# Kernel optimization log

Hardware: AMD Instinct MI355X
Metric: run time of the kernel (lower is better)

Reference implementation:

```python
import jax, jax.numpy as jnp
import numpy as np

B, SQ, SK, D, H = 4, 2048, 2048, 1024, 16
EPS = 1e-6  # flax LayerNorm default


def layer_norm(x, g, b):
    m = x.mean(-1, keepdims=True)
    var = ((x - m) ** 2).mean(-1, keepdims=True)
    return (x - m) * jax.lax.rsqrt(var + EPS) * g + b


def setup_inputs() -> dict:
    key = jax.random.key(0)
    ks = jax.random.split(key, 16)
    s = 1.0 / np.sqrt(D).astype(np.float32)
    inp = {
        'q': jax.random.normal(ks[0], (B, SQ, D), jnp.float32),
        'k': jax.random.normal(ks[1], (B, SK, D), jnp.float32),
        'v': jax.random.normal(ks[2], (B, SK, D), jnp.float32),
        'mask': jax.random.randint(ks[3], (B, SK), 0, 2).astype(bool),
        'Wq': jax.random.normal(ks[4], (D, D), jnp.float32) * s,
        'bq': jnp.zeros((D,), jnp.float32),
        'Wk': jax.random.normal(ks[5], (D, D), jnp.float32) * s,
        'bk': jnp.zeros((D,), jnp.float32),
        'Wv': jax.random.normal(ks[6], (D, D), jnp.float32) * s,
        'bv': jnp.zeros((D,), jnp.float32),
        'Wo': jax.random.normal(ks[7], (D, D), jnp.float32) * s,
        'bo': jnp.zeros((D,), jnp.float32),
        'g1': jnp.ones((D,), jnp.float32),
        'b1': jnp.zeros((D,), jnp.float32),
        'g2': jnp.ones((D,), jnp.float32),
        'b2': jnp.zeros((D,), jnp.float32),
    }
    return inp


def reference(q, k, v, mask, Wq, bq, Wk, bk, Wv, bv, Wo, bo, g1, b1, g2, b2):
    qp = q @ Wq + bq                      # [B, SQ, D]
    kp = k @ Wk + bk                      # [B, SK, D]
    vp = v @ Wv + bv
    qh = qp.reshape(B, SQ, H, D // H)     # head = slice of last dim (matches scatter)
    kh = kp.reshape(B, SK, H, D // H)
    vh = vp.reshape(B, SK, H, D // H)
    # NOTE: original scales by sqrt(dim_out) (full dim), not head dim
    logits = jnp.einsum('bqhd,bkhd->bhqk', qh, kh) / np.sqrt(D).astype(np.float32)
    m = mask[:, None, None, :]            # [B,1,1,SK] broadcast over heads & queries
    A = jax.nn.softmax(jnp.where(m, logits, -jnp.inf), axis=-1)
    A = jnp.where(jnp.isnan(A), 0.0, A)   # fully-masked rows -> 0 (as in original)
    attn = jnp.einsum('bhqk,bkhd->bqhd', A, vh).reshape(B, SQ, D)  # gather heads
    x = layer_norm(qp + attn, g1, b1)
    out = layer_norm(x + jax.nn.relu(x @ Wo + bo), g2, b2)
    return out
```

## Files before the change

kernel.cpp:

```cpp
#include <hip/hip_runtime.h>

#define B_   4
#define SQS  2048
#define SKS  2048
#define DM   1024
#define H_   16
#define MT   8192

typedef __attribute__((ext_vector_type(8))) short bf16x8;
typedef __attribute__((ext_vector_type(4))) float f32x4;

__device__ __forceinline__ float bf2f(unsigned int u) { return __uint_as_float(u << 16); }
__device__ __forceinline__ unsigned short f2bf(float f) {
  unsigned int u = __float_as_uint(f);
  return (unsigned short)((u + 0x7fffu + ((u >> 16) & 1u)) >> 16);
}
__device__ __forceinline__ unsigned int pk_trunc(float a, float b) {
  return __builtin_amdgcn_perm(__float_as_uint(b), __float_as_uint(a), 0x07060302u);
}
__device__ __forceinline__ float fexp2(float x) {
#if __has_builtin(__builtin_amdgcn_exp2f)
  return __builtin_amdgcn_exp2f(x);
#else
  return __expf(x * 0.69314718056f);
#endif
}
__device__ __forceinline__ void async16(const void* g, void* l) {
  __builtin_amdgcn_global_load_lds((const __attribute__((address_space(1))) unsigned int*)g,
                                   (__attribute__((address_space(3))) unsigned int*)l,
                                   16, 0, 0);
}

#define KSCALE 0.0450842200f
#define BIAS_UNMASKED 0.0028151213f

__global__ __launch_bounds__(256)
void cvt3_kernel(const float* __restrict__ a, const float* __restrict__ b,
                 const float* __restrict__ c,
                 unsigned short* __restrict__ oa, unsigned short* __restrict__ ob,
                 unsigned short* __restrict__ oc)
{
  const float* src = (blockIdx.y == 0) ? a : (blockIdx.y == 1) ? b : c;
  unsigned short* dst = (blockIdx.y == 0) ? oa : (blockIdx.y == 1) ? ob : oc;
  size_t i = ((size_t)blockIdx.x * 256 + threadIdx.x) * 4;
  float4 f = *(const float4*)(src + i);
  uint2 o;
  o.x = (unsigned)f2bf(f.x) | ((unsigned)f2bf(f.y) << 16);
  o.y = (unsigned)f2bf(f.z) | ((unsigned)f2bf(f.w) << 16);
  *(uint2*)(dst + i) = o;
}

__global__ __launch_bounds__(256)
void wtrans_kernel(const float* __restrict__ w0, const float* __restrict__ w1,
                   const float* __restrict__ w2, const float* __restrict__ w3,
                   unsigned short* __restrict__ t0, unsigned short* __restrict__ t1,
                   unsigned short* __restrict__ t2, unsigned short* __restrict__ t3)
{
  const float* W = (blockIdx.z == 0) ? w0 : (blockIdx.z == 1) ? w1 : (blockIdx.z == 2) ? w2 : w3;
  unsigned short* Wt = (blockIdx.z == 0) ? t0 : (blockIdx.z == 1) ? t1 : (blockIdx.z == 2) ? t2 : t3;
  __shared__ float s[32][33];
  int n0 = blockIdx.x * 32, k0 = blockIdx.y * 32;
  int tid = threadIdx.x;
#pragma unroll
  for (int p = 0; p < 4; p++) {
    int idx = p * 256 + tid;
    int r = idx >> 5, c = idx & 31;
    s[r][c] = W[(size_t)(k0 + r) * DM + n0 + c];
  }
  __syncthreads();
#pragma unroll
  for (int p = 0; p < 4; p++) {
    int idx = p * 256 + tid;
    int r = idx >> 5, c = idx & 31;
    Wt[(size_t)(n0 + r) * DM + k0 + c] = f2bf(s[c][r]);
  }
}

__global__ __launch_bounds__(256)
void mkbias_kernel(const int* __restrict__ m, float* __restrict__ bias)
{
  int i = blockIdx.x * 256 + threadIdx.x;
  bias[i] = m[i] ? BIAS_UNMASKED : -1e30f;
}

__global__ __launch_bounds__(256)
void qkv_gemm(const unsigned short* __restrict__ A0, const unsigned short* __restrict__ A1,
              const unsigned short* __restrict__ A2,
              const unsigned short* __restrict__ W0, const unsigned short* __restrict__ W1,
              const unsigned short* __restrict__ W2,
              const float* __restrict__ s0, const float* __restrict__ s1,
              const float* __restrict__ s2,
              unsigned short* __restrict__ o0, unsigned short* __restrict__ o1,
              unsigned short* __restrict__ o2)
{
  const int L = blockIdx.x + (blockIdx.y << 3) + (blockIdx.z << 9);
  const int g = L & 7, i5 = L >> 3;
  const int nblk = i5 & 7;
  const int yz = (i5 >> 3) + g * 24;
  const int mblk = yz & 63;
  const int z = yz >> 6;

  const unsigned short* A  = (z == 0) ? A0 : (z == 1) ? A1 : A2;
  const unsigned short* Wt = (z == 0) ? W0 : (z == 1) ? W1 : W2;
  const float* bias        = (z == 0) ? s0 : (z == 1) ? s1 : s2;
  unsigned short* C        = (z == 0) ? o0 : (z == 1) ? o1 : o2;
  const float sc           = (z == 1) ? KSCALE : 1.0f;

  __shared__ short As[128 * 64];
  __shared__ short Bs[128 * 64];
  const int tid = threadIdx.x;
  const int m0 = mblk * 128, n0 = nblk * 128;
  const int wave = tid >> 6, ln = tid & 15, qd = (tid & 63) >> 4;
  const int wm = (wave >> 1) * 64, wn = (wave & 1) * 64;

  int srow[4], sgj[4];
#pragma unroll
  for (int u = 0; u < 4; u++) {
    int c = u * 256 + tid;
    srow[u] = c >> 3;
    sgj[u] = ((c & 7) ^ (srow[u] & 7)) * 8;
  }

  f32x4 acc[4][4];
  const f32x4 vzero = {0.f, 0.f, 0.f, 0.f};
#pragma unroll
  for (int i = 0; i < 4; i++)
#pragma unroll
    for (int j = 0; j < 4; j++) acc[i][j] = vzero;

  for (int k0 = 0; k0 < DM; k0 += 64) {
    __syncthreads();
#pragma unroll
    for (int u = 0; u < 4; u++) {
      int c = u * 256 + tid;
      async16(A  + (size_t)(m0 + srow[u]) * DM + k0 + sgj[u], (char*)As + c * 16);
      async16(Wt + (size_t)(n0 + srow[u]) * DM + k0 + sgj[u], (char*)Bs + c * 16);
    }
    __syncthreads();

#pragma unroll
    for (int kk = 0; kk < 2; kk++) {
      const int ch = ((kk * 4 + qd) ^ (ln & 7)) * 8;
      bf16x8 af[4], bfr[4];
#pragma unroll
      for (int i = 0; i < 4; i++)
        af[i] = *(const bf16x8*)(As + (wm + i * 16 + ln) * 64 + ch);
#pragma unroll
      for (int j = 0; j < 4; j++)
        bfr[j] = *(const bf16x8*)(Bs + (wn + j * 16 + ln) * 64 + ch);
#pragma unroll
      for (int i = 0; i < 4; i++)
#pragma unroll
        for (int j = 0; j < 4; j++)
          acc[i][j] = __builtin_amdgcn_mfma_f32_16x16x32_bf16(af[i], bfr[j], acc[i][j], 0, 0, 0);
    }
  }

#pragma unroll
  for (int j = 0; j < 4; j++) {
    int col = n0 + wn + j * 16 + ln;
    float bj = bias[col];
#pragma unroll
    for (int i = 0; i < 4; i++) {
      int row = m0 + wm + i * 16 + qd * 4;
#pragma unroll
      for (int r = 0; r < 4; r++)
        C[(size_t)(row + r) * DM + col] = f2bf((acc[i][j][r] + bj) * sc);
    }
  }
}

__global__ __launch_bounds__(256)
void gemm_bf16(const unsigned short* __restrict__ A,
               const unsigned short* __restrict__ Wt,
               const float* __restrict__ bias,
               unsigned short* __restrict__ C,
               int relu)
{
  const int L = blockIdx.x + (blockIdx.y << 3);
  const int g = L & 7, i5 = L >> 3;
  const int nblk = i5 & 7;
  const int mblk = (i5 >> 3) + (g << 3);

  __shared__ short As[128 * 64];
  __shared__ short Bs[128 * 64];
  const int tid = threadIdx.x;
  const int m0 = mblk * 128, n0 = nblk * 128;
  const int wave = tid >> 6, ln = tid & 15, qd = (tid & 63) >> 4;
  const int wm = (wave >> 1) * 64, wn = (wave & 1) * 64;

  int srow[4], sgj[4];
#pragma unroll
  for (int u = 0; u < 4; u++) {
    int c = u * 256 + tid;
    srow[u] = c >> 3;
    sgj[u] = ((c & 7) ^ (srow[u] & 7)) * 8;
  }

  f32x4 acc[4][4];
  const f32x4 vzero = {0.f, 0.f, 0.f, 0.f};
#pragma unroll
  for (int i = 0; i < 4; i++)
#pragma unroll
    for (int j = 0; j < 4; j++) acc[i][j] = vzero;

  for (int k0 = 0; k0 < DM; k0 += 64) {
    __syncthreads();
#pragma unroll
    for (int u = 0; u < 4; u++) {
      int c = u * 256 + tid;
      async16(A  + (size_t)(m0 + srow[u]) * DM + k0 + sgj[u], (char*)As + c * 16);
      async16(Wt + (size_t)(n0 + srow[u]) * DM + k0 + sgj[u], (char*)Bs + c * 16);
    }
    __syncthreads();

#pragma unroll
    for (int kk = 0; kk < 2; kk++) {
      const int ch = ((kk * 4 + qd) ^ (ln & 7)) * 8;
      bf16x8 af[4], bfr[4];
#pragma unroll
      for (int i = 0; i < 4; i++)
        af[i] = *(const bf16x8*)(As + (wm + i * 16 + ln) * 64 + ch);
#pragma unroll
      for (int j = 0; j < 4; j++)
        bfr[j] = *(const bf16x8*)(Bs + (wn + j * 16 + ln) * 64 + ch);
#pragma unroll
      for (int i = 0; i < 4; i++)
#pragma unroll
        for (int j = 0; j < 4; j++)
          acc[i][j] = __builtin_amdgcn_mfma_f32_16x16x32_bf16(af[i], bfr[j], acc[i][j], 0, 0, 0);
    }
  }

#pragma unroll
  for (int j = 0; j < 4; j++) {
    int col = n0 + wn + j * 16 + ln;
    float bj = bias[col];
#pragma unroll
    for (int i = 0; i < 4; i++) {
      int row = m0 + wm + i * 16 + qd * 4;
#pragma unroll
      for (int r = 0; r < 4; r++) {
        float v = acc[i][j][r] + bj;
        if (relu) v = fmaxf(v, 0.f);
        C[(size_t)(row + r) * DM + col] = f2bf(v);
      }
    }
  }
}

__global__ __launch_bounds__(256)
void vtrans_kernel(const unsigned short* __restrict__ vp, unsigned short* __restrict__ vT)
{
  __shared__ unsigned short s[64][68];
  int b = blockIdx.z, h = blockIdx.y, k0 = blockIdx.x * 64;
  int tid = threadIdx.x;
#pragma unroll
  for (int p = 0; p < 4; p++) {
    int c = p * 256 + tid;
    int k = c >> 4, d0 = (c & 15) * 4;
    uint2 u = *(const uint2*)(vp + (size_t)(b * SKS + k0 + k) * DM + (h << 6) + d0);
    *(uint2*)(&s[k][d0]) = u;
  }
  __syncthreads();
#pragma unroll
  for (int p = 0; p < 4; p++) {
    int c = p * 256 + tid;
    int d = c >> 4, m = c & 15;
    int t  = ((m & 1) << 1) | (m >> 3);
    int qd = (m >> 1) & 3;
    int ks = t * 16 + qd * 4;
    unsigned short r0 = s[ks + 0][d];
    unsigned short r1 = s[ks + 1][d];
    unsigned short r2 = s[ks + 2][d];
    unsigned short r3 = s[ks + 3][d];
    uint2 u;
    u.x = (unsigned)r0 | ((unsigned)r1 << 16);
    u.y = (unsigned)r2 | ((unsigned)r3 << 16);
    *(uint2*)(vT + (size_t)((b * H_ + h) * 64 + d) * SKS + k0 + m * 4) = u;
  }
}

__global__ __launch_bounds__(256, 4)
void attn_fwd(const unsigned short* __restrict__ qp,
              const unsigned short* __restrict__ kp,
              const unsigned short* __restrict__ vT,
              const float* __restrict__ maskb,
              unsigned short* __restrict__ attn)
{
  __shared__ short Ks[128 * 64];
  __shared__ short Vs[64 * 128];
  __shared__ float bias_s[128];

  const int tid = threadIdx.x;
  const int L = blockIdx.x + (blockIdx.y << 4) + (blockIdx.z << 8);
  const int g = L & 7, i5 = L >> 3;
  const int qblk = i5 & 15;
  const int bh = (i5 >> 4) + (g << 3);
  const int h = bh & 15, b = bh >> 4;
  const int q0 = qblk * 128;
  const int wave = tid >> 6, ln = tid & 15, qd = (tid & 63) >> 4;

  int kRow[4], kOff[4], vRow[4], vOff[4];
#pragma unroll
  for (int u = 0; u < 4; u++) {
    int c = u * 256 + tid;
    kRow[u] = c >> 3;
    kOff[u] = ((c & 7) ^ (kRow[u] & 7)) * 8;
    vRow[u] = c >> 4;
    int j = c & 15;
    vOff[u] = ((j & 8) | ((j ^ vRow[u]) & 7)) * 8;
  }

  const unsigned short* kbase = kp + (size_t)(b * SKS) * DM + (h << 6);
  const unsigned short* vbase = vT + (size_t)((b * H_ + h) * 64) * SKS;

  const unsigned short* qrow = qp + (size_t)(b * SQS + q0 + wave * 32 + ln) * DM + (h << 6);
  bf16x8 qf[2][2];
  qf[0][0] = *(const bf16x8*)(qrow + qd * 8);
  qf[0][1] = *(const bf16x8*)(qrow + 32 + qd * 8);
  qf[1][0] = *(const bf16x8*)(qrow + 16 * DM + qd * 8);
  qf[1][1] = *(const bf16x8*)(qrow + 16 * DM + 32 + qd * 8);

  union { bf16x8 v; unsigned int u[4]; } onesf;
  onesf.u[0] = onesf.u[1] = onesf.u[2] = onesf.u[3] = 0x3F803F80u;

  const f32x4 vzero = {0.f, 0.f, 0.f, 0.f};
  f32x4 oA[2][4], lacc[2];
#pragma unroll
  for (int g2 = 0; g2 < 2; g2++) {
    lacc[g2] = vzero;
#pragma unroll
    for (int t = 0; t < 4; t++) oA[g2][t] = vzero;
  }

  for (int kt = 0; kt < SKS / 128; kt++) {
    const int k0 = kt * 128;
    __syncthreads();
    if (tid < 128) bias_s[tid] = maskb[b * SKS + k0 + tid];
#pragma unroll
    for (int u = 0; u < 4; u++) {
      int c = u * 256 + tid;
      async16(kbase + (size_t)(k0 + kRow[u]) * DM + kOff[u], (char*)Ks + c * 16);
      async16(vbase + (size_t)vRow[u] * SKS + k0 + vOff[u], (char*)Vs + c * 16);
    }
    __syncthreads();

#pragma unroll
    for (int h2 = 0; h2 < 2; h2++) {
      f32x4 sS[2][4];
#pragma unroll
      for (int t = 0; t < 4; t++) {
        const short* krow = Ks + (h2 * 64 + t * 16 + ln) * 64;
        bf16x8 kf0 = *(const bf16x8*)(krow + ((0 + qd) ^ (ln & 7)) * 8);
        bf16x8 kf1 = *(const bf16x8*)(krow + ((4 + qd) ^ (ln & 7)) * 8);
        f32x4 btv = *(const f32x4*)(bias_s + h2 * 64 + t * 16 + qd * 4);
        f32x4 a0 = __builtin_amdgcn_mfma_f32_16x16x32_bf16(kf0, qf[0][0], btv, 0, 0, 0);
        a0       = __builtin_amdgcn_mfma_f32_16x16x32_bf16(kf1, qf[0][1], a0,  0, 0, 0);
        f32x4 a1 = __builtin_amdgcn_mfma_f32_16x16x32_bf16(kf0, qf[1][0], btv, 0, 0, 0);
        a1       = __builtin_amdgcn_mfma_f32_16x16x32_bf16(kf1, qf[1][1], a1,  0, 0, 0);
        sS[0][t] = a0;
        sS[1][t] = a1;
      }

      bf16x8 pf[2][2];
#pragma unroll
      for (int g2 = 0; g2 < 2; g2++) {
        float p[4][4];
#pragma unroll
        for (int t = 0; t < 4; t++) {
          p[t][0] = fexp2(sS[g2][t][0]);
          p[t][1] = fexp2(sS[g2][t][1]);
          p[t][2] = fexp2(sS[g2][t][2]);
          p[t][3] = fexp2(sS[g2][t][3]);
        }
        union { bf16x8 v; unsigned int u[4]; } P0, P1;
        P0.u[0] = pk_trunc(p[0][0], p[0][1]);
        P0.u[1] = pk_trunc(p[0][2], p[0][3]);
        P0.u[2] = pk_trunc(p[2][0], p[2][1]);
        P0.u[3] = pk_trunc(p[2][2], p[2][3]);
        P1.u[0] = pk_trunc(p[1][0], p[1][1]);
        P1.u[1] = pk_trunc(p[1][2], p[1][3]);
        P1.u[2] = pk_trunc(p[3][0], p[3][1]);
        P1.u[3] = pk_trunc(p[3][2], p[3][3]);
        pf[g2][0] = P0.v;
        pf[g2][1] = P1.v;
        lacc[g2] = __builtin_amdgcn_mfma_f32_16x16x32_bf16(pf[g2][0], onesf.v, lacc[g2], 0, 0, 0);
        lacc[g2] = __builtin_amdgcn_mfma_f32_16x16x32_bf16(pf[g2][1], onesf.v, lacc[g2], 0, 0, 0);
      }

#pragma unroll
      for (int t2 = 0; t2 < 4; t2++) {
        const short* vrow = Vs + (t2 * 16 + ln) * 128;
#pragma unroll
        for (int kk = 0; kk < 2; kk++) {
          bf16x8 vf = *(const bf16x8*)(vrow + (h2 * 8 + ((kk * 4 + qd) ^ (ln & 7))) * 8);
          oA[0][t2] = __builtin_amdgcn_mfma_f32_16x16x32_bf16(pf[0][kk], vf, oA[0][t2], 0, 0, 0);
          oA[1][t2] = __builtin_amdgcn_mfma_f32_16x16x32_bf16(pf[1][kk], vf, oA[1][t2], 0, 0, 0);
        }
      }
    }
  }

#pragma unroll
  for (int g2 = 0; g2 < 2; g2++) {
    float linv[4];
#pragma unroll
    for (int r = 0; r < 4; r++)
      linv[r] = (lacc[g2][r] > 0.f) ? 1.0f / lacc[g2][r] : 0.f;
#pragma unroll
    for (int t2 = 0; t2 < 4; t2++)
#pragma unroll
      for (int r = 0; r < 4; r++) {
        size_t idx = (size_t)(b * SQS + q0 + wave * 32 + g2 * 16 + qd * 4 + r) * DM
                   + (h << 6) + t2 * 16 + ln;
        attn[idx] = f2bf(oA[g2][t2][r] * linv[r]);
      }
  }
}

__global__ __launch_bounds__(256)
void ln_fuse(const unsigned short* __restrict__ Xa, const unsigned short* __restrict__ Xb,
             const float* __restrict__ gamma, const float* __restrict__ beta,
             unsigned short* __restrict__ outb, float* __restrict__ outf, int mode)
{
  const int row = blockIdx.x, tid = threadIdx.x;
  const size_t base = (size_t)row * DM + tid * 4;
  uint2 ua = *(const uint2*)(Xa + base);
  uint2 ub = *(const uint2*)(Xb + base);
  float v0 = bf2f(ua.x & 0xffffu) + bf2f(ub.x & 0xffffu);
  float v1 = bf2f(ua.x >> 16)     + bf2f(ub.x >> 16);
  float v2 = bf2f(ua.y & 0xffffu) + bf2f(ub.y & 0xffffu);
  float v3 = bf2f(ua.y >> 16)     + bf2f(ub.y >> 16);
  float s  = (v0 + v1) + (v2 + v3);
  float s2 = (v0 * v0 + v1 * v1) + (v2 * v2 + v3 * v3);
#pragma unroll
  for (int off = 1; off < 64; off <<= 1) {
    s  += __shfl_xor(s, off);
    s2 += __shfl_xor(s2, off);
  }
  __shared__ float red[8];
  if ((tid & 63) == 0) { red[tid >> 6] = s; red[4 + (tid >> 6)] = s2; }
  __syncthreads();
  float S  = (red[0] + red[1]) + (red[2] + red[3]);
  float S2 = (red[4] + red[5]) + (red[6] + red[7]);
  float mean = S * (1.0f / 1024.0f);
  float var  = S2 * (1.0f / 1024.0f) - mean * mean;
  float rstd = rsqrtf(var + 1e-6f);
  int c = tid * 4;
  float o0 = (v0 - mean) * rstd * gamma[c + 0] + beta[c + 0];
  float o1 = (v1 - mean) * rstd * gamma[c + 1] + beta[c + 1];
  float o2 = (v2 - mean) * rstd * gamma[c + 2] + beta[c + 2];
  float o3 = (v3 - mean) * rstd * gamma[c + 3] + beta[c + 3];
  if (mode == 0) {
    uint2 o;
    o.x = (unsigned)f2bf(o0) | ((unsigned)f2bf(o1) << 16);
    o.y = (unsigned)f2bf(o2) | ((unsigned)f2bf(o3) << 16);
    *(uint2*)(outb + base) = o;
  } else {
    float4 o = {o0, o1, o2, o3};
    *(float4*)(outf + base) = o;
  }
}

extern "C" void kernel_launch(void* const* d_in, const int* in_sizes, int n_in,
                              void* d_out, int out_size, void* d_ws, size_t ws_size,
                              hipStream_t stream)
{
  (void)in_sizes; (void)n_in; (void)out_size; (void)ws_size;
  const float* q    = (const float*)d_in[0];
  const float* k    = (const float*)d_in[1];
  const float* v    = (const float*)d_in[2];
  const int*   mask = (const int*)  d_in[3];
  const float* Wq   = (const float*)d_in[4];
  const float* bq   = (const float*)d_in[5];
  const float* Wk   = (const float*)d_in[6];
  const float* bk   = (const float*)d_in[7];
  const float* Wv   = (const float*)d_in[8];
  const float* bv   = (const float*)d_in[9];
  const float* Wo   = (const float*)d_in[10];
  const float* bo   = (const float*)d_in[11];
  const float* g1   = (const float*)d_in[12];
  const float* b1   = (const float*)d_in[13];
  const float* g2   = (const float*)d_in[14];
  const float* b2   = (const float*)d_in[15];

  char* ws = (char*)d_ws;
  const size_t SZ16 = (size_t)16 << 20;
  unsigned short* qi   = (unsigned short*)(ws + 0 * SZ16);
  unsigned short* ki   = (unsigned short*)(ws + 1 * SZ16);
  unsigned short* vi   = (unsigned short*)(ws + 2 * SZ16);
  unsigned short* qpb  = (unsigned short*)(ws + 3 * SZ16);
  unsigned short* kpb  = (unsigned short*)(ws + 4 * SZ16);
  unsigned short* vpb  = (unsigned short*)(ws + 5 * SZ16);
  unsigned short* vTb  = (unsigned short*)(ws + 6 * SZ16);
  unsigned short* Wqt  = (unsigned short*)(ws + 7 * SZ16 + ((size_t)0 << 20));
  unsigned short* Wkt  = (unsigned short*)(ws + 7 * SZ16 + ((size_t)2 << 20));
  unsigned short* Wvt  = (unsigned short*)(ws + 7 * SZ16 + ((size_t)4 << 20));
  unsigned short* Wot  = (unsigned short*)(ws + 7 * SZ16 + ((size_t)6 << 20));
  float*          mskb = (float*)         (ws + 7 * SZ16 + ((size_t)8 << 20));
  unsigned short* attnb = qi;
  unsigned short* xb    = ki;
  unsigned short* hb    = vi;

  cvt3_kernel  <<<dim3(8192, 3),    256, 0, stream>>>(q, k, v, qi, ki, vi);
  wtrans_kernel<<<dim3(32, 32, 4),  256, 0, stream>>>(Wq, Wk, Wv, Wo, Wqt, Wkt, Wvt, Wot);
  mkbias_kernel<<<32,               256, 0, stream>>>(mask, mskb);

  qkv_gemm     <<<dim3(8, 64, 3),   256, 0, stream>>>(qi, ki, vi, Wqt, Wkt, Wvt,
                                                      bq, bk, bv, qpb, kpb, vpb);

  vtrans_kernel<<<dim3(32, 16, 4),  256, 0, stream>>>(vpb, vTb);
  attn_fwd     <<<dim3(16, 16, 4),  256, 0, stream>>>(qpb, kpb, vTb, mskb, attnb);

  ln_fuse      <<<8192,             256, 0, stream>>>(qpb, attnb, g1, b1, xb, nullptr, 0);
  gemm_bf16    <<<dim3(8, 64),      256, 0, stream>>>(xb, Wot, bo, hb, 1);
  ln_fuse      <<<8192,             256, 0, stream>>>(xb, hb, g2, b2, nullptr, (float*)d_out, 1);
}
```

Before: 359.5 us.

## Merge prep kernels, fuse V transpose into QKV GEMM, double attention query tile

New measurement: 347.4 us. -3.4%, faster.

```diff
diff --git a/kernel.cpp b/kernel.cpp
--- a/kernel.cpp
+++ b/kernel.cpp
@@ -15,6 +15,10 @@
   unsigned int u = __float_as_uint(f);
   return (unsigned short)((u + 0x7fffu + ((u >> 16) & 1u)) >> 16);
 }
+__device__ __forceinline__ unsigned int pk_bf16(float a, float b) {
+  return __builtin_amdgcn_perm(__float_as_uint(b) + 0x8000u,
+                               __float_as_uint(a) + 0x8000u, 0x07060302u);
+}
 __device__ __forceinline__ unsigned int pk_trunc(float a, float b) {
   return __builtin_amdgcn_perm(__float_as_uint(b), __float_as_uint(a), 0x07060302u);
 }
@@ -35,52 +39,51 @@
 #define BIAS_UNMASKED 0.0028151213f
 
 __global__ __launch_bounds__(256)
-void cvt3_kernel(const float* __restrict__ a, const float* __restrict__ b,
-                 const float* __restrict__ c,
-                 unsigned short* __restrict__ oa, unsigned short* __restrict__ ob,
-                 unsigned short* __restrict__ oc)
+void prep_all(const float* __restrict__ q, const float* __restrict__ k,
+              const float* __restrict__ v, const int* __restrict__ mask,
+              const float* __restrict__ Wq, const float* __restrict__ Wk,
+              const float* __restrict__ Wv, const float* __restrict__ Wo,
+              unsigned short* __restrict__ qi, unsigned short* __restrict__ ki,
+              unsigned short* __restrict__ vi,
+              unsigned short* __restrict__ Wqt, unsigned short* __restrict__ Wkt,
+              unsigned short* __restrict__ Wvt, unsigned short* __restrict__ Wot,
+              float* __restrict__ mskb)
 {
-  const float* src = (blockIdx.y == 0) ? a : (blockIdx.y == 1) ? b : c;
-  unsigned short* dst = (blockIdx.y == 0) ? oa : (blockIdx.y == 1) ? ob : oc;
-  size_t i = ((size_t)blockIdx.x * 256 + threadIdx.x) * 4;
-  float4 f = *(const float4*)(src + i);
-  uint2 o;
-  o.x = (unsigned)f2bf(f.x) | ((unsigned)f2bf(f.y) << 16);
-  o.y = (unsigned)f2bf(f.z) | ((unsigned)f2bf(f.w) << 16);
-  *(uint2*)(dst + i) = o;
-}
-
-__global__ __launch_bounds__(256)
-void wtrans_kernel(const float* __restrict__ w0, const float* __restrict__ w1,
-                   const float* __restrict__ w2, const float* __restrict__ w3,
-                   unsigned short* __restrict__ t0, unsigned short* __restrict__ t1,
-                   unsigned short* __restrict__ t2, unsigned short* __restrict__ t3)
-{
-  const float* W = (blockIdx.z == 0) ? w0 : (blockIdx.z == 1) ? w1 : (blockIdx.z == 2) ? w2 : w3;
-  unsigned short* Wt = (blockIdx.z == 0) ? t0 : (blockIdx.z == 1) ? t1 : (blockIdx.z == 2) ? t2 : t3;
   __shared__ float s[32][33];
-  int n0 = blockIdx.x * 32, k0 = blockIdx.y * 32;
-  int tid = threadIdx.x;
-#pragma unroll
-  for (int p = 0; p < 4; p++) {
-    int idx = p * 256 + tid;
-    int r = idx >> 5, c = idx & 31;
-    s[r][c] = W[(size_t)(k0 + r) * DM + n0 + c];
-  }
-  __syncthreads();
-#pragma unroll
-  for (int p = 0; p < 4; p++) {
-    int idx = p * 256 + tid;
-    int r = idx >> 5, c = idx & 31;
-    Wt[(size_t)(n0 + r) * DM + k0 + c] = f2bf(s[c][r]);
-  }
-}
-
-__global__ __launch_bounds__(256)
-void mkbias_kernel(const int* __restrict__ m, float* __restrict__ bias)
-{
-  int i = blockIdx.x * 256 + threadIdx.x;
-  bias[i] = m[i] ? BIAS_UNMASKED : -1e30f;
+  const int bx = blockIdx.x, tid = threadIdx.x;
+  if (bx < 24576) {
+    const int which = bx >> 13, i = bx & 8191;
+    const float* src = (which == 0) ? q : (which == 1) ? k : v;
+    unsigned short* dst = (which == 0) ? qi : (which == 1) ? ki : vi;
+    size_t o = ((size_t)i * 256 + tid) * 4;
+    float4 f = *(const float4*)(src + o);
+    uint2 u;
+    u.x = pk_bf16(f.x, f.y);
+    u.y = pk_bf16(f.z, f.w);
+    *(uint2*)(dst + o) = u;
+  } else if (bx < 28672) {
+    const int idx = bx - 24576;
+    const int w = idx >> 10, t = idx & 1023;
+    const int n0 = (t & 31) * 32, k0 = (t >> 5) * 32;
+    const float* W = (w == 0) ? Wq : (w == 1) ? Wk : (w == 2) ? Wv : Wo;
+    unsigned short* Wt = (w == 0) ? Wqt : (w == 1) ? Wkt : (w == 2) ? Wvt : Wot;
+#pragma unroll
+    for (int p = 0; p < 4; p++) {
+      int c = p * 256 + tid;
+      int r = c >> 5, cc = c & 31;
+      s[r][cc] = W[(size_t)(k0 + r) * DM + n0 + cc];
+    }
+    __syncthreads();
+#pragma unroll
+    for (int p = 0; p < 4; p++) {
+      int c = p * 256 + tid;
+      int r = c >> 5, cc = c & 31;
+      Wt[(size_t)(n0 + r) * DM + k0 + cc] = f2bf(s[cc][r]);
+    }
+  } else {
+    int i = (bx - 28672) * 256 + tid;
+    mskb[i] = mask[i] ? BIAS_UNMASKED : -1e30f;
+  }
 }
 
 __global__ __launch_bounds__(256)
@@ -91,7 +94,7 @@
               const float* __restrict__ s0, const float* __restrict__ s1,
               const float* __restrict__ s2,
               unsigned short* __restrict__ o0, unsigned short* __restrict__ o1,
-              unsigned short* __restrict__ o2)
+              unsigned short* __restrict__ vT)
 {
   const int L = blockIdx.x + (blockIdx.y << 3) + (blockIdx.z << 9);
   const int g = L & 7, i5 = L >> 3;
@@ -103,8 +106,6 @@
   const unsigned short* A  = (z == 0) ? A0 : (z == 1) ? A1 : A2;
   const unsigned short* Wt = (z == 0) ? W0 : (z == 1) ? W1 : W2;
   const float* bias        = (z == 0) ? s0 : (z == 1) ? s1 : s2;
-  unsigned short* C        = (z == 0) ? o0 : (z == 1) ? o1 : o2;
-  const float sc           = (z == 1) ? KSCALE : 1.0f;
 
   __shared__ short As[128 * 64];
   __shared__ short Bs[128 * 64];
@@ -156,16 +157,37 @@
     }
   }
 
-#pragma unroll
-  for (int j = 0; j < 4; j++) {
-    int col = n0 + wn + j * 16 + ln;
-    float bj = bias[col];
-#pragma unroll
-    for (int i = 0; i < 4; i++) {
-      int row = m0 + wm + i * 16 + qd * 4;
-#pragma unroll
-      for (int r = 0; r < 4; r++)
-        C[(size_t)(row + r) * DM + col] = f2bf((acc[i][j][r] + bj) * sc);
+  if (z != 2) {
+    unsigned short* C = (z == 0) ? o0 : o1;
+    const float sc = (z == 1) ? KSCALE : 1.0f;
+#pragma unroll
+    for (int j = 0; j < 4; j++) {
+      int col = n0 + wn + j * 16 + ln;
+      float bj = bias[col];
+#pragma unroll
+      for (int i = 0; i < 4; i++) {
+        int row = m0 + wm + i * 16 + qd * 4;
+#pragma unroll
+        for (int r = 0; r < 4; r++)
+          C[(size_t)(row + r) * DM + col] = f2bf((acc[i][j][r] + bj) * sc);
+      }
+    }
+  } else {
+#pragma unroll
+    for (int j = 0; j < 4; j++) {
+      int col = n0 + wn + j * 16 + ln;
+      int h = col >> 6, d = col & 63;
+      float bj = bias[col];
+#pragma unroll
+      for (int i = 0; i < 4; i++) {
+        int tok0 = m0 + wm + i * 16 + qd * 4;
+        int bb = tok0 >> 11;
+        int kcol = ((tok0 & 2047) & ~63) + (i & 1) * 32 + qd * 8 + ((i >> 1) & 1) * 4;
+        uint2 u;
+        u.x = pk_bf16(acc[i][j][0] + bj, acc[i][j][1] + bj);
+        u.y = pk_bf16(acc[i][j][2] + bj, acc[i][j][3] + bj);
+        *(uint2*)(vT + ((size_t)(bb * H_ + h) * 64 + d) * SKS + kcol) = u;
+      }
     }
   }
 }
@@ -249,39 +271,7 @@
   }
 }
 
-__global__ __launch_bounds__(256)
-void vtrans_kernel(const unsigned short* __restrict__ vp, unsigned short* __restrict__ vT)
-{
-  __shared__ unsigned short s[64][68];
-  int b = blockIdx.z, h = blockIdx.y, k0 = blockIdx.x * 64;
-  int tid = threadIdx.x;
-#pragma unroll
-  for (int p = 0; p < 4; p++) {
-    int c = p * 256 + tid;
-    int k = c >> 4, d0 = (c & 15) * 4;
-    uint2 u = *(const uint2*)(vp + (size_t)(b * SKS + k0 + k) * DM + (h << 6) + d0);
-    *(uint2*)(&s[k][d0]) = u;
-  }
-  __syncthreads();
-#pragma unroll
-  for (int p = 0; p < 4; p++) {
-    int c = p * 256 + tid;
-    int d = c >> 4, m = c & 15;
-    int t  = ((m & 1) << 1) | (m >> 3);
-    int qd = (m >> 1) & 3;
-    int ks = t * 16 + qd * 4;
-    unsigned short r0 = s[ks + 0][d];
-    unsigned short r1 = s[ks + 1][d];
-    unsigned short r2 = s[ks + 2][d];
-    unsigned short r3 = s[ks + 3][d];
-    uint2 u;
-    u.x = (unsigned)r0 | ((unsigned)r1 << 16);
-    u.y = (unsigned)r2 | ((unsigned)r3 << 16);
-    *(uint2*)(vT + (size_t)((b * H_ + h) * 64 + d) * SKS + k0 + m * 4) = u;
-  }
-}
-
-__global__ __launch_bounds__(256, 4)
+__global__ __launch_bounds__(256, 2)
 void attn_fwd(const unsigned short* __restrict__ qp,
               const unsigned short* __restrict__ kp,
               const unsigned short* __restrict__ vT,
@@ -293,12 +283,12 @@
   __shared__ float bias_s[128];
 
   const int tid = threadIdx.x;
-  const int L = blockIdx.x + (blockIdx.y << 4) + (blockIdx.z << 8);
+  const int L = blockIdx.x + (blockIdx.y << 3) + (blockIdx.z << 7);
   const int g = L & 7, i5 = L >> 3;
-  const int qblk = i5 & 15;
-  const int bh = (i5 >> 4) + (g << 3);
+  const int qblk = i5 & 7;
+  const int bh = (i5 >> 3) + (g << 3);
   const int h = bh & 15, b = bh >> 4;
-  const int q0 = qblk * 128;
+  const int q0 = qblk * 256;
   const int wave = tid >> 6, ln = tid & 15, qd = (tid & 63) >> 4;
 
   int kRow[4], kOff[4], vRow[4], vOff[4];
@@ -315,23 +305,25 @@
   const unsigned short* kbase = kp + (size_t)(b * SKS) * DM + (h << 6);
   const unsigned short* vbase = vT + (size_t)((b * H_ + h) * 64) * SKS;
 
-  const unsigned short* qrow = qp + (size_t)(b * SQS + q0 + wave * 32 + ln) * DM + (h << 6);
-  bf16x8 qf[2][2];
-  qf[0][0] = *(const bf16x8*)(qrow + qd * 8);
-  qf[0][1] = *(const bf16x8*)(qrow + 32 + qd * 8);
-  qf[1][0] = *(const bf16x8*)(qrow + 16 * DM + qd * 8);
-  qf[1][1] = *(const bf16x8*)(qrow + 16 * DM + 32 + qd * 8);
+  bf16x8 qf[4][2];
+#pragma unroll
+  for (int gq = 0; gq < 4; gq++) {
+    const unsigned short* qrow =
+        qp + (size_t)(b * SQS + q0 + wave * 64 + gq * 16 + ln) * DM + (h << 6);
+    qf[gq][0] = *(const bf16x8*)(qrow + qd * 8);
+    qf[gq][1] = *(const bf16x8*)(qrow + 32 + qd * 8);
+  }
 
   union { bf16x8 v; unsigned int u[4]; } onesf;
   onesf.u[0] = onesf.u[1] = onesf.u[2] = onesf.u[3] = 0x3F803F80u;
 
   const f32x4 vzero = {0.f, 0.f, 0.f, 0.f};
-  f32x4 oA[2][4], lacc[2];
-#pragma unroll
-  for (int g2 = 0; g2 < 2; g2++) {
-    lacc[g2] = vzero;
-#pragma unroll
-    for (int t = 0; t < 4; t++) oA[g2][t] = vzero;
+  f32x4 oA[4][4], lacc[4];
+#pragma unroll
+  for (int gq = 0; gq < 4; gq++) {
+    lacc[gq] = vzero;
+#pragma unroll
+    for (int t = 0; t < 4; t++) oA[gq][t] = vzero;
   }
 
   for (int kt = 0; kt < SKS / 128; kt++) {
@@ -348,31 +340,32 @@
 
 #pragma unroll
     for (int h2 = 0; h2 < 2; h2++) {
-      f32x4 sS[2][4];
+      bf16x8 kf[4][2];
+      f32x4 btv[4];
 #pragma unroll
       for (int t = 0; t < 4; t++) {
         const short* krow = Ks + (h2 * 64 + t * 16 + ln) * 64;
-        bf16x8 kf0 = *(const bf16x8*)(krow + ((0 + qd) ^ (ln & 7)) * 8);
-        bf16x8 kf1 = *(const bf16x8*)(krow + ((4 + qd) ^ (ln & 7)) * 8);
-        f32x4 btv = *(const f32x4*)(bias_s + h2 * 64 + t * 16 + qd * 4);
-        f32x4 a0 = __builtin_amdgcn_mfma_f32_16x16x32_bf16(kf0, qf[0][0], btv, 0, 0, 0);
-        a0       = __builtin_amdgcn_mfma_f32_16x16x32_bf16(kf1, qf[0][1], a0,  0, 0, 0);
-        f32x4 a1 = __builtin_amdgcn_mfma_f32_16x16x32_bf16(kf0, qf[1][0], btv, 0, 0, 0);
-        a1       = __builtin_amdgcn_mfma_f32_16x16x32_bf16(kf1, qf[1][1], a1,  0, 0, 0);
-        sS[0][t] = a0;
-        sS[1][t] = a1;
-      }
-
-      bf16x8 pf[2][2];
-#pragma unroll
-      for (int g2 = 0; g2 < 2; g2++) {
+        kf[t][0] = *(const bf16x8*)(krow + ((0 + qd) ^ (ln & 7)) * 8);
+        kf[t][1] = *(const bf16x8*)(krow + ((4 + qd) ^ (ln & 7)) * 8);
+        btv[t] = *(const f32x4*)(bias_s + h2 * 64 + t * 16 + qd * 4);
+      }
+
+      bf16x8 pf[4][2];
+#pragma unroll
+      for (int gq = 0; gq < 4; gq++) {
+        f32x4 sS[4];
+#pragma unroll
+        for (int t = 0; t < 4; t++) {
+          f32x4 a = __builtin_amdgcn_mfma_f32_16x16x32_bf16(kf[t][0], qf[gq][0], btv[t], 0, 0, 0);
+          sS[t]   = __builtin_amdgcn_mfma_f32_16x16x32_bf16(kf[t][1], qf[gq][1], a,      0, 0, 0);
+        }
         float p[4][4];
 #pragma unroll
         for (int t = 0; t < 4; t++) {
-          p[t][0] = fexp2(sS[g2][t][0]);
-          p[t][1] = fexp2(sS[g2][t][1]);
-          p[t][2] = fexp2(sS[g2][t][2]);
-          p[t][3] = fexp2(sS[g2][t][3]);
+          p[t][0] = fexp2(sS[t][0]);
+          p[t][1] = fexp2(sS[t][1]);
+          p[t][2] = fexp2(sS[t][2]);
+          p[t][3] = fexp2(sS[t][3]);
         }
         union { bf16x8 v; unsigned int u[4]; } P0, P1;
         P0.u[0] = pk_trunc(p[0][0], p[0][1]);
@@ -383,38 +376,39 @@
         P1.u[1] = pk_trunc(p[1][2], p[1][3]);
         P1.u[2] = pk_trunc(p[3][0], p[3][1]);
         P1.u[3] = pk_trunc(p[3][2], p[3][3]);
-        pf[g2][0] = P0.v;
-        pf[g2][1] = P1.v;
-        lacc[g2] = __builtin_amdgcn_mfma_f32_16x16x32_bf16(pf[g2][0], onesf.v, lacc[g2], 0, 0, 0);
-        lacc[g2] = __builtin_amdgcn_mfma_f32_16x16x32_bf16(pf[g2][1], onesf.v, lacc[g2], 0, 0, 0);
+        pf[gq][0] = P0.v;
+        pf[gq][1] = P1.v;
+        lacc[gq] = __builtin_amdgcn_mfma_f32_16x16x32_bf16(pf[gq][0], onesf.v, lacc[gq], 0, 0, 0);
+        lacc[gq] = __builtin_amdgcn_mfma_f32_16x16x32_bf16(pf[gq][1], onesf.v, lacc[gq], 0, 0, 0);
       }
 
 #pragma unroll
       for (int t2 = 0; t2 < 4; t2++) {
         const short* vrow = Vs + (t2 * 16 + ln) * 128;
-#pragma unroll
-        for (int kk = 0; kk < 2; kk++) {
-          bf16x8 vf = *(const bf16x8*)(vrow + (h2 * 8 + ((kk * 4 + qd) ^ (ln & 7))) * 8);
-          oA[0][t2] = __builtin_amdgcn_mfma_f32_16x16x32_bf16(pf[0][kk], vf, oA[0][t2], 0, 0, 0);
-          oA[1][t2] = __builtin_amdgcn_mfma_f32_16x16x32_bf16(pf[1][kk], vf, oA[1][t2], 0, 0, 0);
+        bf16x8 vf0 = *(const bf16x8*)(vrow + (h2 * 8 + ((0 + qd) ^ (ln & 7))) * 8);
+        bf16x8 vf1 = *(const bf16x8*)(vrow + (h2 * 8 + ((4 + qd) ^ (ln & 7))) * 8);
+#pragma unroll
+        for (int gq = 0; gq < 4; gq++) {
+          oA[gq][t2] = __builtin_amdgcn_mfma_f32_16x16x32_bf16(pf[gq][0], vf0, oA[gq][t2], 0, 0, 0);
+          oA[gq][t2] = __builtin_amdgcn_mfma_f32_16x16x32_bf16(pf[gq][1], vf1, oA[gq][t2], 0, 0, 0);
         }
       }
     }
   }
 
 #pragma unroll
-  for (int g2 = 0; g2 < 2; g2++) {
+  for (int gq = 0; gq < 4; gq++) {
     float linv[4];
 #pragma unroll
     for (int r = 0; r < 4; r++)
-      linv[r] = (lacc[g2][r] > 0.f) ? 1.0f / lacc[g2][r] : 0.f;
+      linv[r] = (lacc[gq][r] > 0.f) ? 1.0f / lacc[gq][r] : 0.f;
 #pragma unroll
     for (int t2 = 0; t2 < 4; t2++)
 #pragma unroll
       for (int r = 0; r < 4; r++) {
-        size_t idx = (size_t)(b * SQS + q0 + wave * 32 + g2 * 16 + qd * 4 + r) * DM
+        size_t idx = (size_t)(b * SQS + q0 + wave * 64 + gq * 16 + qd * 4 + r) * DM
                    + (h << 6) + t2 * 16 + ln;
-        attn[idx] = f2bf(oA[g2][t2][r] * linv[r]);
+        attn[idx] = f2bf(oA[gq][t2][r] * linv[r]);
       }
   }
 }
@@ -492,7 +486,6 @@
   unsigned short* vi   = (unsigned short*)(ws + 2 * SZ16);
   unsigned short* qpb  = (unsigned short*)(ws + 3 * SZ16);
   unsigned short* kpb  = (unsigned short*)(ws + 4 * SZ16);
-  unsigned short* vpb  = (unsigned short*)(ws + 5 * SZ16);
   unsigned short* vTb  = (unsigned short*)(ws + 6 * SZ16);
   unsigned short* Wqt  = (unsigned short*)(ws + 7 * SZ16 + ((size_t)0 << 20));
   unsigned short* Wkt  = (unsigned short*)(ws + 7 * SZ16 + ((size_t)2 << 20));
@@ -503,15 +496,13 @@
   unsigned short* xb    = ki;
   unsigned short* hb    = vi;
 
-  cvt3_kernel  <<<dim3(8192, 3),    256, 0, stream>>>(q, k, v, qi, ki, vi);
-  wtrans_kernel<<<dim3(32, 32, 4),  256, 0, stream>>>(Wq, Wk, Wv, Wo, Wqt, Wkt, Wvt, Wot);
-  mkbias_kernel<<<32,               256, 0, stream>>>(mask, mskb);
+  prep_all     <<<28704,            256, 0, stream>>>(q, k, v, mask, Wq, Wk, Wv, Wo,
+                                                      qi, ki, vi, Wqt, Wkt, Wvt, Wot, mskb);
 
   qkv_gemm     <<<dim3(8, 64, 3),   256, 0, stream>>>(qi, ki, vi, Wqt, Wkt, Wvt,
-                                                      bq, bk, bv, qpb, kpb, vpb);
-
-  vtrans_kernel<<<dim3(32, 16, 4),  256, 0, stream>>>(vpb, vTb);
-  attn_fwd     <<<dim3(16, 16, 4),  256, 0, stream>>>(qpb, kpb, vTb, mskb, attnb);
+                                                      bq, bk, bv, qpb, kpb, vTb);
+
+  attn_fwd     <<<dim3(8, 16, 4),   256, 0, stream>>>(qpb, kpb, vTb, mskb, attnb);
 
   ln_fuse      <<<8192,             256, 0, stream>>>(qpb, attnb, g1, b1, xb, nullptr, 0);
   gemm_bf16    <<<dim3(8, 64),      256, 0, stream>>>(xb, Wot, bo, hb, 1);
```
